# Performance work log

Hardware: AMD Instinct MI355X
Metric: run time of the kernel (lower is better)

## Reference

```python
import jax, jax.numpy as jnp
import numpy as np

B, T, C, K, L = 32, 4096, 8, 64, 100000
EPS = 1e-12


def _fit_quantile_edges(flat):
    # flat: [L, C] numpy. Faithful to GroupTokenizer._fit_quantile (vectorized over channels).
    idx = np.floor(np.arange(K + 1) * (L - 1) / K).astype(np.int64)
    idx = np.clip(idx, None, L - 1)
    vals = np.sort(flat, axis=0)            # [L, C] sorted per channel
    l = vals[idx[:K]].T.copy()              # [C, K]; l[:,0] = vals[idx[0]] = min
    r = vals[idx[1:]].T.copy()              # [C, K]
    l[:, 0] = vals[0]                       # mn
    r[:, -1] = vals[-1]                     # mx
    return l.astype(np.float32), r.astype(np.float32)


def setup_inputs() -> dict:
    key = jax.random.key(0)
    k1, _ = jax.random.split(key)
    rng = np.random.default_rng(0)
    flat = rng.normal(size=(L, C)).astype(np.float32)
    l, r = _fit_quantile_edges(flat)
    y = jax.random.normal(k1, (B, T, C), dtype=jnp.float32)
    return {"y": y, "left_edges": jnp.asarray(l), "right_edges": jnp.asarray(r)}


def reference(y, left_edges, right_edges):
    # y: [B, T, C]; edges: [C, K]
    k = left_edges.shape[-1]
    yk = y[..., None]                                   # [B,T,C,1]
    in_bin = (yk >= left_edges) & (yk < right_edges)    # [B,T,C,K]
    has_bin = in_bin.any(axis=-1)                       # [B,T,C]
    labels = jnp.argmax(in_bin, axis=-1)                # [B,T,C]
    labels = jnp.where(has_bin, labels, k - 1)
    cidx = jnp.arange(left_edges.shape[0])              # [C]
    left_sel = left_edges[cidx, labels]                 # [B,T,C]
    right_sel = right_edges[cidx, labels]               # [B,T,C]
    width = jnp.maximum(right_sel - left_sel, EPS)
    delta = jnp.clip((y - left_sel) / width, 0.0, 1.0)  # [B,T,C]
    onehot = labels[..., None] == jnp.arange(k)         # [B,T,C,K]
    reg = jnp.where(onehot, delta[..., None], jnp.asarray(-1.0, y.dtype))
    return labels, reg
```

## Files before the change

### kernel.cpp

```cpp
#include <hip/hip_runtime.h>

#define N_ELEM (32 * 4096 * 8)
#define CCH 8
#define KB 64

typedef float vfloat4 __attribute__((ext_vector_type(4)));

__global__ __launch_bounds__(256) void group_tokenizer_kernel(
    const float* __restrict__ y,
    const float* __restrict__ le,
    const float* __restrict__ re,
    float* __restrict__ out,
    int ngroups) {
  __shared__ float ls[CCH][KB + 1];
  __shared__ float rs[CCH][KB + 1];
  const int tid = threadIdx.x;
  for (int t = tid; t < CCH * KB; t += blockDim.x) {
    ls[t >> 6][t & 63] = le[t];
    rs[t >> 6][t & 63] = re[t];
  }
  __syncthreads();

  const int lane = tid & 63;
  const int wid = tid >> 6;
  const int wavesPerBlock = blockDim.x >> 6;
  const int gwave = blockIdx.x * wavesPerBlock + wid;
  const int nwaves = gridDim.x * wavesPerBlock;

  const vfloat4 neg1 = {-1.0f, -1.0f, -1.0f, -1.0f};

  for (int g = gwave; g < ngroups; g += nwaves) {
    const int e = g * 64 + lane;
    const float yv = y[e];

    float* regbase = out + (size_t)N_ELEM + (size_t)g * (64 * KB);
    vfloat4* regv = (vfloat4*)regbase;
#pragma unroll
    for (int j = 0; j < 16; ++j) {
      regv[(j << 6) + lane] = neg1;
    }

    const int c = e & (CCH - 1);
    const float* lr = ls[c];
    const float* rr = rs[c];

    int lo = 0, hi = KB;
#pragma unroll
    for (int it = 0; it < 7; ++it) {
      const int mid = (lo + hi) >> 1;
      const bool cond = yv < rr[mid];
      hi = cond ? mid : hi;
      lo = cond ? lo : mid + 1;
    }
    const int label = (lo < KB && yv >= lr[lo]) ? lo : (KB - 1);

    const float left = lr[label];
    const float right = rr[label];
    const float width = fmaxf(right - left, 1e-12f);
    float delta = (yv - left) / width;
    delta = fminf(fmaxf(delta, 0.0f), 1.0f);

    out[e] = (float)label;

    asm volatile("s_waitcnt vmcnt(0)" ::: "memory");

    regbase[(lane << 6) + label] = delta;
  }
}

extern "C" void kernel_launch(void* const* d_in, const int* in_sizes, int n_in,
                              void* d_out, int out_size, void* d_ws, size_t ws_size,
                              hipStream_t stream) {
  const float* y = (const float*)d_in[0];
  const float* le = (const float*)d_in[1];
  const float* re = (const float*)d_in[2];
  float* out = (float*)d_out;

  const int n = in_sizes[0];
  const int ngroups = n / 64;
  const int wavesPerBlock = 4;
  const int groupsPerWave = 2;
  const int blocks =
      (ngroups + wavesPerBlock * groupsPerWave - 1) / (wavesPerBlock * groupsPerWave);

  group_tokenizer_kernel<<<blocks, 256, 0, stream>>>(y, le, re, out, ngroups);
}
```

Before: 281.3 us.

## Split -1 fill into separate kernel and scatter deltas in second pass

The single fused kernel, which filled each group's reg block with -1 and then waited on vmcnt before scattering the delta, becomes two kernels. A grid-stride fill kernel writes -1 over the whole reg region, then a label/scatter kernel computes labels and writes the single delta per element. This removes the per-iteration s_waitcnt stall and the mixed fill/compute loop. In exchange the scatter writes land in a separate pass after the fill, which adds a second launch and may touch cache lines again.

```diff
diff --git a/kernel.cpp b/kernel.cpp
--- a/kernel.cpp
+++ b/kernel.cpp
@@ -6,7 +6,17 @@
 
 typedef float vfloat4 __attribute__((ext_vector_type(4)));
 
-__global__ __launch_bounds__(256) void group_tokenizer_kernel(
+__global__ __launch_bounds__(256) void reg_fill_kernel(float* __restrict__ out,
+                                                       long nvec4) {
+  const vfloat4 neg1 = {-1.0f, -1.0f, -1.0f, -1.0f};
+  vfloat4* v = (vfloat4*)(out + (size_t)N_ELEM);
+  const long stride = (long)gridDim.x * blockDim.x;
+  for (long i = (long)blockIdx.x * blockDim.x + threadIdx.x; i < nvec4; i += stride) {
+    v[i] = neg1;
+  }
+}
+
+__global__ __launch_bounds__(256) void label_scatter_kernel(
     const float* __restrict__ y,
     const float* __restrict__ le,
     const float* __restrict__ re,
@@ -27,22 +37,13 @@
   const int gwave = blockIdx.x * wavesPerBlock + wid;
   const int nwaves = gridDim.x * wavesPerBlock;
 
-  const vfloat4 neg1 = {-1.0f, -1.0f, -1.0f, -1.0f};
+  const int c = lane & (CCH - 1);
+  const float* lr = ls[c];
+  const float* rr = rs[c];
 
   for (int g = gwave; g < ngroups; g += nwaves) {
     const int e = g * 64 + lane;
     const float yv = y[e];
-
-    float* regbase = out + (size_t)N_ELEM + (size_t)g * (64 * KB);
-    vfloat4* regv = (vfloat4*)regbase;
-#pragma unroll
-    for (int j = 0; j < 16; ++j) {
-      regv[(j << 6) + lane] = neg1;
-    }
-
-    const int c = e & (CCH - 1);
-    const float* lr = ls[c];
-    const float* rr = rs[c];
 
     int lo = 0, hi = KB;
 #pragma unroll
@@ -55,16 +56,13 @@
     const int label = (lo < KB && yv >= lr[lo]) ? lo : (KB - 1);
 
     const float left = lr[label];
-    const float right = rr[label];
-    const float width = fmaxf(right - left, 1e-12f);
+    const float width = fmaxf(rr[label] - left, 1e-12f);
     float delta = (yv - left) / width;
     delta = fminf(fmaxf(delta, 0.0f), 1.0f);
 
     out[e] = (float)label;
 
-    asm volatile("s_waitcnt vmcnt(0)" ::: "memory");
-
-    regbase[(lane << 6) + label] = delta;
+    out[(size_t)N_ELEM + (size_t)g * (64 * KB) + (size_t)lane * KB + label] = delta;
   }
 }
 
@@ -78,10 +76,9 @@
 
   const int n = in_sizes[0];
   const int ngroups = n / 64;
-  const int wavesPerBlock = 4;
-  const int groupsPerWave = 2;
-  const int blocks =
-      (ngroups + wavesPerBlock * groupsPerWave - 1) / (wavesPerBlock * groupsPerWave);
+  const long nvec4 = (long)ngroups * (64 * KB) / 4;
 
-  group_tokenizer_kernel<<<blocks, 256, 0, stream>>>(y, le, re, out, ngroups);
+  reg_fill_kernel<<<1024, 256, 0, stream>>>(out, nvec4);
+
+  label_scatter_kernel<<<4096, 256, 0, stream>>>(y, le, re, out, ngroups);
 }
```

New measurement: 300.6 us. 6.9% more time.
